# Optimization experiments

Hardware: AMD Instinct MI355X
Metric: run time of the kernel (lower is better)

Reference implementation:

```python
import jax, jax.numpy as jnp
import numpy as np

KERNEL = 500
PAD_IDX = 256


def setup_inputs() -> dict:
    key = jax.random.key(0)
    ks = jax.random.split(key, 8)
    B, L = 8, 1_000_000
    x = jax.random.randint(ks[0], (B, L), 0, 257, dtype=jnp.int64)
    emb = jax.random.normal(ks[1], (257, 8), dtype=jnp.float32)
    emb = emb.at[PAD_IDX].set(0.0)  # padding_idx row is zero
    W1 = jax.random.normal(ks[2], (128, 8, KERNEL), dtype=jnp.float32) * 0.02
    b1 = jax.random.normal(ks[3], (128,), dtype=jnp.float32) * 0.02
    W2 = jax.random.normal(ks[4], (128, 8, KERNEL), dtype=jnp.float32) * 0.02
    b2 = jax.random.normal(ks[5], (128,), dtype=jnp.float32) * 0.02
    fcW = jax.random.normal(ks[6], (2, 128), dtype=jnp.float32) * 0.1
    fcb = jax.random.normal(ks[7], (2,), dtype=jnp.float32) * 0.1
    return {"x": x, "emb": emb, "W1": W1, "b1": b1, "W2": W2, "b2": b2, "fcW": fcW, "fcb": fcb}


def reference(x, emb, W1, b1, W2, b2, fcW, fcb):
    B, L = x.shape
    P = L // KERNEL  # non-overlapping patches (stride == kernel_size)
    # embedding with padding_idx semantics: output zero at pad positions
    e = emb[x] * (x != PAD_IDX)[..., None].astype(emb.dtype)  # [B, L, 8]
    patches = e.reshape(B, P, KERNEL, 8)                      # [B, P, K, C]
    # conv1d(k=stride=500) == patchified GEMM; weight layout [out, in, k]
    g1 = jnp.einsum('bpkc,ock->bpo', patches, W1) + b1        # [B, P, 128]
    g2 = jnp.einsum('bpkc,ock->bpo', patches, W2) + b2
    h = jax.nn.relu(g1 * jax.nn.sigmoid(g2))                  # GLU gate + relu
    m = jnp.max(h, axis=1)                                    # global max pool -> [B, 128]
    return m @ fcW.T + fcb                                    # [B, num_classes]
```

## Files before the change

kernel.cpp:

```cpp
#include <hip/hip_runtime.h>


typedef __attribute__((ext_vector_type(8))) short short8;
typedef __attribute__((ext_vector_type(4))) float f32x4;

__device__ __forceinline__ unsigned short f2b(float f) {
    union { float f; unsigned u; } un;
    un.f = f;
    unsigned u = un.u;
    return (unsigned short)((u + 0x7FFFu + ((u >> 16) & 1u)) >> 16);
}

#define KT_COUNT 125
#define WS_BBLK_BYTES (KT_COUNT * 256 * 32 * 2)
#define WS_MWS_OFF WS_BBLK_BYTES

__global__ __launch_bounds__(256) void prep_weights(
        const float* __restrict__ W1, const float* __restrict__ W2,
        unsigned short* __restrict__ Bblk, float* __restrict__ m_ws) {
    int u   = blockIdx.x * 256 + threadIdx.x;
    int kt  = u >> 10;
    int rem = u & 1023;
    int c   = rem >> 2;
    int g   = rem & 3;
    int k   = kt * 4 + g;
    int grp = c >> 5, s = c & 31;
    const float* W = (s < 16) ? W1 : W2;
    int oo = grp * 16 + (s & 15);
    unsigned short v[8];
#pragma unroll
    for (int ch = 0; ch < 8; ++ch) v[ch] = f2b(W[oo * 4000 + ch * 500 + k]);
    uint4 pack;
    pack.x = (unsigned)v[0] | ((unsigned)v[1] << 16);
    pack.y = (unsigned)v[2] | ((unsigned)v[3] << 16);
    pack.z = (unsigned)v[4] | ((unsigned)v[5] << 16);
    pack.w = (unsigned)v[6] | ((unsigned)v[7] << 16);
    *(uint4*)&Bblk[u * 8] = pack;
    if (blockIdx.x < 4) m_ws[blockIdx.x * 256 + threadIdx.x] = 0.f;
}

__global__ __launch_bounds__(64, 1) void malconv_main(
        const int* __restrict__ x, const float* __restrict__ emb,
        const float* __restrict__ b1, const float* __restrict__ b2,
        const unsigned short* __restrict__ Bblk, float* __restrict__ m_ws) {
    __shared__ __align__(16) unsigned short embb[257 * 8];

    const int t = threadIdx.x;
    for (int e = t; e < 257 * 8; e += 64) embb[e] = f2b(emb[e]);

    const int w  = (blockIdx.x & 7) * 125 + (blockIdx.x >> 3);
    const int mt = w >> 2, nq = w & 3;
    const int m0 = mt * 64;

    const int quad = t >> 4, l16 = t & 15;

    const unsigned short* bbase = Bblk + (nq * 64 + l16) * 32 + quad * 8;

    const int* xr = x + (m0 + l16) * 500 + quad;

    f32x4 acc[4][4];
#pragma unroll
    for (int mi = 0; mi < 4; ++mi)
#pragma unroll
        for (int ni = 0; ni < 4; ++ni) {
            f32x4 z = {0.f, 0.f, 0.f, 0.f};
            acc[mi][ni] = z;
        }

    __syncthreads();

    short8 a0[4], a1[4], a2[4];
    short8 q0[4], q1[4], q2[4];
    int    x0[4], x1[4], x2[4];

#pragma unroll
    for (int mi = 0; mi < 4; ++mi) {
        int v0 = xr[mi * 8000 + 0];
        int v1 = xr[mi * 8000 + 4];
        int v2 = xr[mi * 8000 + 8];
        a0[mi] = *(const short8*)&embb[v0 * 8];
        a1[mi] = *(const short8*)&embb[v1 * 8];
        a2[mi] = *(const short8*)&embb[v2 * 8];
        x0[mi] = xr[mi * 8000 + 12];
        x1[mi] = xr[mi * 8000 + 16];
        x2[mi] = xr[mi * 8000 + 20];
    }
#pragma unroll
    for (int ni = 0; ni < 4; ++ni) {
        q0[ni] = *(const short8*)(bbase + 0 * 8192 + ni * 512);
        q1[ni] = *(const short8*)(bbase + 1 * 8192 + ni * 512);
        q2[ni] = *(const short8*)(bbase + 2 * 8192 + ni * 512);
    }

    auto phase = [&](short8 (&A)[4], short8 (&B)[4], int (&X)[4], int kt) {
#pragma unroll
        for (int mi = 0; mi < 4; ++mi)
#pragma unroll
            for (int ni = 0; ni < 4; ++ni)
                acc[mi][ni] = __builtin_amdgcn_mfma_f32_16x16x32_bf16(
                    A[mi], B[ni], acc[mi][ni], 0, 0, 0);
        const int ktn = (kt + 3 < KT_COUNT) ? kt + 3 : KT_COUNT - 1;
#pragma unroll
        for (int ni = 0; ni < 4; ++ni)
            B[ni] = *(const short8*)(bbase + ktn * 8192 + ni * 512);
#pragma unroll
        for (int mi = 0; mi < 4; ++mi)
            A[mi] = *(const short8*)&embb[X[mi] * 8];
        const int ktx = (kt + 6 < KT_COUNT) ? kt + 6 : KT_COUNT - 1;
#pragma unroll
        for (int mi = 0; mi < 4; ++mi)
            X[mi] = xr[mi * 8000 + ktx * 4];
    };

    for (int ktb = 0; ktb < 123; ktb += 3) {
        phase(a0, q0, x0, ktb);
        phase(a1, q1, x1, ktb + 1);
        phase(a2, q2, x2, ktb + 2);
    }
#pragma unroll
    for (int mi = 0; mi < 4; ++mi)
#pragma unroll
        for (int ni = 0; ni < 4; ++ni)
            acc[mi][ni] = __builtin_amdgcn_mfma_f32_16x16x32_bf16(
                a0[mi], q0[ni], acc[mi][ni], 0, 0, 0);
#pragma unroll
    for (int mi = 0; mi < 4; ++mi)
#pragma unroll
        for (int ni = 0; ni < 4; ++ni)
            acc[mi][ni] = __builtin_amdgcn_mfma_f32_16x16x32_bf16(
                a1[mi], q1[ni], acc[mi][ni], 0, 0, 0);

    const int b0i = m0 / 2000;
    const int bsplit = (b0i + 1) * 2000;
    const bool crosses = (m0 + 63) >= bsplit;
#pragma unroll
    for (int p = 0; p < 2; ++p) {
        const int j = nq * 32 + p * 16 + l16;
        const float bb1 = b1[j], bb2 = b2[j];
        float mx0 = 0.f, mx1 = 0.f;
#pragma unroll
        for (int mi = 0; mi < 4; ++mi)
#pragma unroll
            for (int r = 0; r < 4; ++r) {
                int row = m0 + mi * 16 + quad * 4 + r;
                float g1 = acc[mi][2 * p][r] + bb1;
                float g2 = acc[mi][2 * p + 1][r] + bb2;
                float h = fmaxf(g1 / (1.f + __expf(-g2)), 0.f);
                if (row >= bsplit) mx1 = fmaxf(mx1, h);
                else               mx0 = fmaxf(mx0, h);
            }
        mx0 = fmaxf(mx0, __shfl_xor(mx0, 16));
        mx0 = fmaxf(mx0, __shfl_xor(mx0, 32));
        mx1 = fmaxf(mx1, __shfl_xor(mx1, 16));
        mx1 = fmaxf(mx1, __shfl_xor(mx1, 32));
        if (quad == 0) {
            atomicMax((int*)&m_ws[b0i * 128 + j], __float_as_int(mx0));
            if (crosses)
                atomicMax((int*)&m_ws[(b0i + 1) * 128 + j], __float_as_int(mx1));
        }
    }
}

__global__ void fc_kernel(const float* __restrict__ m_ws,
                          const float* __restrict__ fcW,
                          const float* __restrict__ fcb,
                          float* __restrict__ out) {
    int t = threadIdx.x;
    if (t < 16) {
        int b = t >> 1, j = t & 1;
        float s = 0.f;
        for (int o = 0; o < 128; ++o) s += m_ws[b * 128 + o] * fcW[j * 128 + o];
        out[t] = s + fcb[j];
    }
}

extern "C" void kernel_launch(void* const* d_in, const int* in_sizes, int n_in,
                              void* d_out, int out_size, void* d_ws, size_t ws_size,
                              hipStream_t stream) {
    const int*   x   = (const int*)d_in[0];
    const float* emb = (const float*)d_in[1];
    const float* W1  = (const float*)d_in[2];
    const float* b1  = (const float*)d_in[3];
    const float* W2  = (const float*)d_in[4];
    const float* b2  = (const float*)d_in[5];
    const float* fcW = (const float*)d_in[6];
    const float* fcb = (const float*)d_in[7];
    float* out = (float*)d_out;

    unsigned short* Bblk = (unsigned short*)d_ws;
    float* m_ws = (float*)((char*)d_ws + WS_MWS_OFF);

    prep_weights<<<500, 256, 0, stream>>>(W1, W2, Bblk, m_ws);
    malconv_main<<<1000, 64, 0, stream>>>(x, emb, b1, b2, Bblk, m_ws);
    fc_kernel<<<1, 64, 0, stream>>>(m_ws, fcW, fcb, out);
}
```

Baseline: 159.8 us.

## Stage token indices into LDS via async global_load_lds, vectorize weight prep

The main kernel no longer fetches token ids straight into registers with a deep register pipeline. It now stages 32-position chunks of each row's token ids into a double-buffered LDS array using global_load_lds, then reads them from LDS for the embedding lookups. The B-fragment prefetch depth drops from three to two stages. The weight-prep kernel now reads W with float4 loads and writes four k-slices per thread, using fewer blocks. The aim is to cut register pressure and the latency of scattered index loads. The cost is extra barriers, and it relies on the async LDS loads being complete at each barrier.

```diff
diff --git a/kernel.cpp b/kernel.cpp
--- a/kernel.cpp
+++ b/kernel.cpp
@@ -11,6 +11,12 @@
     return (unsigned short)((u + 0x7FFFu + ((u >> 16) & 1u)) >> 16);
 }
 
+__device__ __forceinline__ void gll4(const int* g, void* l) {
+    __builtin_amdgcn_global_load_lds(
+        (const __attribute__((address_space(1))) void*)g,
+        (__attribute__((address_space(3))) void*)l, 4, 0, 0);
+}
+
 #define KT_COUNT 125
 #define WS_BBLK_BYTES (KT_COUNT * 256 * 32 * 2)
 #define WS_MWS_OFF WS_BBLK_BYTES
@@ -18,24 +24,28 @@
 __global__ __launch_bounds__(256) void prep_weights(
         const float* __restrict__ W1, const float* __restrict__ W2,
         unsigned short* __restrict__ Bblk, float* __restrict__ m_ws) {
-    int u   = blockIdx.x * 256 + threadIdx.x;
-    int kt  = u >> 10;
-    int rem = u & 1023;
-    int c   = rem >> 2;
-    int g   = rem & 3;
-    int k   = kt * 4 + g;
+    int u  = blockIdx.x * 256 + threadIdx.x;
+    int kt = u >> 8;
+    int c  = u & 255;
     int grp = c >> 5, s = c & 31;
     const float* W = (s < 16) ? W1 : W2;
     int oo = grp * 16 + (s & 15);
-    unsigned short v[8];
-#pragma unroll
-    for (int ch = 0; ch < 8; ++ch) v[ch] = f2b(W[oo * 4000 + ch * 500 + k]);
-    uint4 pack;
-    pack.x = (unsigned)v[0] | ((unsigned)v[1] << 16);
-    pack.y = (unsigned)v[2] | ((unsigned)v[3] << 16);
-    pack.z = (unsigned)v[4] | ((unsigned)v[5] << 16);
-    pack.w = (unsigned)v[6] | ((unsigned)v[7] << 16);
-    *(uint4*)&Bblk[u * 8] = pack;
+    unsigned short v[4][8];
+#pragma unroll
+    for (int ch = 0; ch < 8; ++ch) {
+        float4 w4 = *(const float4*)&W[oo * 4000 + ch * 500 + kt * 4];
+        v[0][ch] = f2b(w4.x); v[1][ch] = f2b(w4.y);
+        v[2][ch] = f2b(w4.z); v[3][ch] = f2b(w4.w);
+    }
+#pragma unroll
+    for (int g = 0; g < 4; ++g) {
+        uint4 pack;
+        pack.x = (unsigned)v[g][0] | ((unsigned)v[g][1] << 16);
+        pack.y = (unsigned)v[g][2] | ((unsigned)v[g][3] << 16);
+        pack.z = (unsigned)v[g][4] | ((unsigned)v[g][5] << 16);
+        pack.w = (unsigned)v[g][6] | ((unsigned)v[g][7] << 16);
+        *(uint4*)&Bblk[u * 32 + g * 8] = pack;
+    }
     if (blockIdx.x < 4) m_ws[blockIdx.x * 256 + threadIdx.x] = 0.f;
 }
 
@@ -44,6 +54,7 @@
         const float* __restrict__ b1, const float* __restrict__ b2,
         const unsigned short* __restrict__ Bblk, float* __restrict__ m_ws) {
     __shared__ __align__(16) unsigned short embb[257 * 8];
+    __shared__ __align__(16) int xs[2][32][64];
 
     const int t = threadIdx.x;
     for (int e = t; e < 257 * 8; e += 64) embb[e] = f2b(emb[e]);
@@ -56,7 +67,17 @@
 
     const unsigned short* bbase = Bblk + (nq * 64 + l16) * 32 + quad * 8;
 
-    const int* xr = x + (m0 + l16) * 500 + quad;
+    const int* xrow = x + (m0 + t) * 500;
+
+    auto stage = [&](int Sn) {
+        int* dst0 = &xs[Sn & 1][0][0];
+#pragma unroll
+        for (int p = 0; p < 32; ++p) {
+            int pe = Sn * 32 + p;
+            if (pe > 499) pe = 499;
+            gll4(xrow + pe, (void*)(dst0 + p * 64));
+        }
+    };
 
     f32x4 acc[4][4];
 #pragma unroll
@@ -67,68 +88,52 @@
             acc[mi][ni] = z;
         }
 
+    stage(0);
     __syncthreads();
 
-    short8 a0[4], a1[4], a2[4];
-    short8 q0[4], q1[4], q2[4];
-    int    x0[4], x1[4], x2[4];
-
-#pragma unroll
-    for (int mi = 0; mi < 4; ++mi) {
-        int v0 = xr[mi * 8000 + 0];
-        int v1 = xr[mi * 8000 + 4];
-        int v2 = xr[mi * 8000 + 8];
-        a0[mi] = *(const short8*)&embb[v0 * 8];
-        a1[mi] = *(const short8*)&embb[v1 * 8];
-        a2[mi] = *(const short8*)&embb[v2 * 8];
-        x0[mi] = xr[mi * 8000 + 12];
-        x1[mi] = xr[mi * 8000 + 16];
-        x2[mi] = xr[mi * 8000 + 20];
-    }
+    short8 bA[4], bB[4];
 #pragma unroll
     for (int ni = 0; ni < 4; ++ni) {
-        q0[ni] = *(const short8*)(bbase + 0 * 8192 + ni * 512);
-        q1[ni] = *(const short8*)(bbase + 1 * 8192 + ni * 512);
-        q2[ni] = *(const short8*)(bbase + 2 * 8192 + ni * 512);
-    }
-
-    auto phase = [&](short8 (&A)[4], short8 (&B)[4], int (&X)[4], int kt) {
+        bA[ni] = *(const short8*)(bbase + 0 * 8192 + ni * 512);
+        bB[ni] = *(const short8*)(bbase + 1 * 8192 + ni * 512);
+    }
+
+    auto step = [&](int kt, int kl, short8 (&B)[4], int cur) {
+        int xv[4];
+        short8 af[4];
+#pragma unroll
+        for (int mi = 0; mi < 4; ++mi)
+            xv[mi] = xs[cur][kl * 4 + quad][mi * 16 + l16];
+#pragma unroll
+        for (int mi = 0; mi < 4; ++mi)
+            af[mi] = *(const short8*)&embb[xv[mi] * 8];
 #pragma unroll
         for (int mi = 0; mi < 4; ++mi)
 #pragma unroll
             for (int ni = 0; ni < 4; ++ni)
                 acc[mi][ni] = __builtin_amdgcn_mfma_f32_16x16x32_bf16(
-                    A[mi], B[ni], acc[mi][ni], 0, 0, 0);
-        const int ktn = (kt + 3 < KT_COUNT) ? kt + 3 : KT_COUNT - 1;
+                    af[mi], B[ni], acc[mi][ni], 0, 0, 0);
+        const int ktn = (kt + 2 < KT_COUNT) ? kt + 2 : KT_COUNT - 1;
 #pragma unroll
         for (int ni = 0; ni < 4; ++ni)
             B[ni] = *(const short8*)(bbase + ktn * 8192 + ni * 512);
-#pragma unroll
-        for (int mi = 0; mi < 4; ++mi)
-            A[mi] = *(const short8*)&embb[X[mi] * 8];
-        const int ktx = (kt + 6 < KT_COUNT) ? kt + 6 : KT_COUNT - 1;
-#pragma unroll
-        for (int mi = 0; mi < 4; ++mi)
-            X[mi] = xr[mi * 8000 + ktx * 4];
     };
 
-    for (int ktb = 0; ktb < 123; ktb += 3) {
-        phase(a0, q0, x0, ktb);
-        phase(a1, q1, x1, ktb + 1);
-        phase(a2, q2, x2, ktb + 2);
-    }
-#pragma unroll
-    for (int mi = 0; mi < 4; ++mi)
-#pragma unroll
-        for (int ni = 0; ni < 4; ++ni)
-            acc[mi][ni] = __builtin_amdgcn_mfma_f32_16x16x32_bf16(
-                a0[mi], q0[ni], acc[mi][ni], 0, 0, 0);
-#pragma unroll
-    for (int mi = 0; mi < 4; ++mi)
-#pragma unroll
-        for (int ni = 0; ni < 4; ++ni)
-            acc[mi][ni] = __builtin_amdgcn_mfma_f32_16x16x32_bf16(
-                a1[mi], q1[ni], acc[mi][ni], 0, 0, 0);
+    for (int S = 0; S < 15; ++S) {
+        stage(S + 1);
+        const int cur = S & 1;
+#pragma unroll
+        for (int kp = 0; kp < 4; ++kp) {
+            step(S * 8 + kp * 2,     kp * 2,     bA, cur);
+            step(S * 8 + kp * 2 + 1, kp * 2 + 1, bB, cur);
+        }
+        __syncthreads();
+    }
+    step(120, 0, bA, 1);
+    step(121, 1, bB, 1);
+    step(122, 2, bA, 1);
+    step(123, 3, bB, 1);
+    step(124, 4, bA, 1);
 
     const int b0i = m0 / 2000;
     const int bsplit = (b0i + 1) * 2000;
@@ -190,7 +195,7 @@
     unsigned short* Bblk = (unsigned short*)d_ws;
     float* m_ws = (float*)((char*)d_ws + WS_MWS_OFF);
 
-    prep_weights<<<500, 256, 0, stream>>>(W1, W2, Bblk, m_ws);
+    prep_weights<<<125, 256, 0, stream>>>(W1, W2, Bblk, m_ws);
     malconv_main<<<1000, 64, 0, stream>>>(x, emb, b1, b2, Bblk, m_ws);
     fc_kernel<<<1, 64, 0, stream>>>(m_ws, fcW, fcb, out);
 }
```

Result: slower. 171.9 us (+7.5%).
